# Performance work log

Hardware: AMD Instinct MI355X
Metric: run time of the kernel (lower is better)

## Reference

```python
import jax, jax.numpy as jnp
import numpy as np

H = 64  # lstm_units
FORGET_BIAS = 1.0  # TF LSTMCell default


def setup_inputs() -> dict:
    key = jax.random.key(0)
    k1, k2, k3 = jax.random.split(key, 3)
    B, T = 256, 2048
    x = jax.random.normal(k1, (B, T, 1), dtype=jnp.float32)
    # Layer 1: LSTMCell(64), input dim 1 -> kernel [(1+64), 4*64]
    W1 = jax.random.normal(k2, (1 + H, 4 * H), dtype=jnp.float32) * 0.1
    b1 = jnp.zeros((4 * H,), dtype=jnp.float32)
    # Layer 2: LSTMCell(1), input dim 64 -> kernel [(64+1), 4*1]
    W2 = jax.random.normal(k3, (H + 1, 4), dtype=jnp.float32) * 0.1
    b2 = jnp.zeros((4,), dtype=jnp.float32)
    return {"x": x, "W1": W1, "b1": b1, "W2": W2, "b2": b2}


def _lstm_step(c, h, xt, W, b):
    # TF LSTMCell: gates from concat([x, h]) @ W + b, order i, j, f, o
    z = jnp.concatenate([xt, h], axis=-1) @ W + b
    i, j, f, o = jnp.split(z, 4, axis=-1)
    c_new = jax.nn.sigmoid(f + FORGET_BIAS) * c + jax.nn.sigmoid(i) * jnp.tanh(j)
    h_new = jax.nn.sigmoid(o) * jnpp_tanh(c_new) if False else jax.nn.sigmoid(o) * jnp.tanh(c_new)
    return c_new, h_new


def reference(x, W1, b1, W2, b2):
    # x: [B, T, 1] -> outputs of 2-layer stacked LSTM, final layer size 1
    B = x.shape[0]

    def step(carry, xt):
        c1, h1, c2, h2 = carry
        c1, h1 = _lstm_step(c1, h1, xt, W1, b1)
        c2, h2 = _lstm_step(c2, h2, h1, W2, b2)
        return (c1, h1, c2, h2), h2

    init = (
        jnp.zeros((B, H), x.dtype),
        jnp.zeros((B, H), x.dtype),
        jnp.zeros((B, 1), x.dtype),
        jnp.zeros((B, 1), x.dtype),
    )
    x_tbf = jnp.swapaxes(x, 0, 1)  # [T, B, 1]
    _, ys = jax.lax.scan(step, init, x_tbf)  # ys: [T, B, 1]
    return jnp.swapaxes(ys, 0, 1)  # [B, T, 1]
```

## Files before the change

### kernel.cpp

```cpp
#include <hip/hip_runtime.h>

constexpr int kT = 2048;
constexpr int kB = 256;
constexpr int kH = 64;

typedef __attribute__((ext_vector_type(2))) float f32x2;
typedef __attribute__((ext_vector_type(4))) float f32x4;

__device__ __forceinline__ float fast_sig(float x) {
    return __builtin_amdgcn_rcpf(1.0f + __expf(-x));
}
__device__ __forceinline__ float fast_tanh(float x) {
    float t = __expf(2.0f * x);
    return 1.0f - 2.0f * __builtin_amdgcn_rcpf(t + 1.0f);
}

__global__ __launch_bounds__(128)
__attribute__((amdgpu_waves_per_eu(1, 1)))
void lstm2_kernel(
    const float* __restrict__ x, const float* __restrict__ W1,
    const float* __restrict__ b1, const float* __restrict__ W2,
    const float* __restrict__ b2, float* __restrict__ out)
{
    __shared__ f32x4 x4_lds[kT / 4];
    __shared__ f32x4 out4_lds[kT / 4];
    __shared__ float h_lds[2][kH];
    __shared__ f32x4 z4_lds[2];
    __shared__ float pad_lds[11128];

    float* x_lds = (float*)x4_lds;
    float* out_lds = (float*)out4_lds;

    const int tid = threadIdx.x;
    const int b = blockIdx.x;
    const int w = tid >> 6;
    const int l = tid & 63;
    const int p = l >> 5;
    const int u = w * 32 + (l & 31);

    const f32x4* xg4 = (const f32x4*)(x + (size_t)b * kT);
    f32x4* outg4 = (f32x4*)(out + (size_t)b * kT);

    for (int i = tid; i < kT / 4; i += 128) x4_lds[i] = xg4[i];
    if (tid < kH) { h_lds[0][tid] = 0.0f; h_lds[1][tid] = 0.0f; }
    if (b == 0x7fffffff) pad_lds[tid] = x[0];

    f32x2 wp[4][16];
    float w0g[4], bg[4];
    const int base = p * 32;
    #pragma unroll
    for (int g = 0; g < 4; ++g) {
        const int col = g * 64 + u;
        w0g[g] = W1[col];
        bg[g]  = b1[col];
        #pragma unroll
        for (int j = 0; j < 16; ++j) {
            wp[g][j].x = W1[(base + 2 * j + 1) * 256 + col];
            wp[g][j].y = W1[(base + 2 * j + 2) * 256 + col];
        }
    }
    const int s = l & 15, gg = l >> 4;
    float w2p0 = W2[(s +  0) * 4 + gg];
    float w2p1 = W2[(s + 16) * 4 + gg];
    float w2p2 = W2[(s + 32) * 4 + gg];
    float w2p3 = W2[(s + 48) * 4 + gg];
    float b2g  = b2[gg];
    f32x4 w2t = ((const f32x4*)W2)[kH];

    #pragma unroll
    for (int g = 0; g < 4; ++g) {
        #pragma unroll
        for (int j = 0; j < 16; ++j) asm volatile("" : "+v"(wp[g][j]));
        asm volatile("" : "+v"(w0g[g]), "+v"(bg[g]));
    }
    asm volatile("" : "+v"(w2p0), "+v"(w2p1), "+v"(w2p2), "+v"(w2p3));
    asm volatile("" : "+v"(w2t), "+v"(b2g));

    float c1 = 0.0f, c2 = 0.0f, h2 = 0.0f;

    __syncthreads();

    #pragma unroll 1
    for (int t = 0; t < kT; ++t) {
        const int cur = t & 1, nxt = cur ^ 1;

        const float xt = x_lds[t];
        f32x4 hp[8];
        const f32x4* hb4 = (const f32x4*)h_lds[cur];
        #pragma unroll
        for (int k = 0; k < 8; ++k) hp[k] = hb4[p * 8 + k];

        if (w == 0) {
            if (t >= 2) {
                const f32x4 z4 = z4_lds[nxt];
                const float zi = z4.x + h2 * w2t.x;
                const float zj = z4.y + h2 * w2t.y;
                const float zf = z4.z + h2 * w2t.z;
                const float zo = z4.w + h2 * w2t.w;
                c2 = fast_sig(zf + 1.0f) * c2 + fast_sig(zi) * fast_tanh(zj);
                h2 = fast_sig(zo) * fast_tanh(c2);
                if (l == 0) out_lds[t - 2] = h2;
            }
        } else {
            const float* hb = h_lds[cur];
            float pr = hb[s] * w2p0;
            pr = fmaf(hb[s + 16], w2p1, pr);
            pr = fmaf(hb[s + 32], w2p2, pr);
            pr = fmaf(hb[s + 48], w2p3, pr);
            pr += __shfl_xor(pr, 1);
            pr += __shfl_xor(pr, 2);
            pr += __shfl_xor(pr, 4);
            pr += __shfl_xor(pr, 8);
            if ((l & 15) == 0) ((float*)&z4_lds[cur])[gg] = pr + b2g;
        }

        f32x2 a0, a1, a2, a3;
        a0.x = (p == 0) ? fmaf(xt, w0g[0], bg[0]) : 0.0f; a0.y = 0.0f;
        a1.x = (p == 0) ? fmaf(xt, w0g[1], bg[1]) : 0.0f; a1.y = 0.0f;
        a2.x = (p == 0) ? fmaf(xt, w0g[2], bg[2]) : 0.0f; a2.y = 0.0f;
        a3.x = (p == 0) ? fmaf(xt, w0g[3], bg[3]) : 0.0f; a3.y = 0.0f;
        #pragma unroll
        for (int k = 0; k < 8; ++k) {
            const f32x2 lo = hp[k].xy;
            const f32x2 hi = hp[k].zw;
            a0 += lo * wp[0][2*k]; a0 += hi * wp[0][2*k+1];
            a1 += lo * wp[1][2*k]; a1 += hi * wp[1][2*k+1];
            a2 += lo * wp[2][2*k]; a2 += hi * wp[2][2*k+1];
            a3 += lo * wp[3][2*k]; a3 += hi * wp[3][2*k+1];
        }
        float zi = a0.x + a0.y; zi += __shfl_xor(zi, 32);
        float zj = a1.x + a1.y; zj += __shfl_xor(zj, 32);
        float zf = a2.x + a2.y; zf += __shfl_xor(zf, 32);
        float zo = a3.x + a3.y; zo += __shfl_xor(zo, 32);
        const float gi = fast_sig(zi);
        const float gj = fast_tanh(zj);
        const float gf = fast_sig(zf + 1.0f);
        const float go = fast_sig(zo);
        c1 = fmaf(gf, c1, gi * gj);
        const float h1n = go * fast_tanh(c1);
        if (p == 0) h_lds[nxt][u] = h1n;

        __syncthreads();
    }

    if (w == 0) {
        {
            const f32x4 z4 = z4_lds[1];
            const float zi = z4.x + h2 * w2t.x;
            const float zj = z4.y + h2 * w2t.y;
            const float zf = z4.z + h2 * w2t.z;
            const float zo = z4.w + h2 * w2t.w;
            c2 = fast_sig(zf + 1.0f) * c2 + fast_sig(zi) * fast_tanh(zj);
            h2 = fast_sig(zo) * fast_tanh(c2);
            if (l == 0) out_lds[kT - 2] = h2;
        }
        {
            const float* hb = h_lds[0];
            float pr = hb[s] * w2p0;
            pr = fmaf(hb[s + 16], w2p1, pr);
            pr = fmaf(hb[s + 32], w2p2, pr);
            pr = fmaf(hb[s + 48], w2p3, pr);
            pr += __shfl_xor(pr, 1);
            pr += __shfl_xor(pr, 2);
            pr += __shfl_xor(pr, 4);
            pr += __shfl_xor(pr, 8);
            const float prb = pr + b2g;
            const float zi = __shfl(prb,  0) + h2 * w2t.x;
            const float zj = __shfl(prb, 16) + h2 * w2t.y;
            const float zf = __shfl(prb, 32) + h2 * w2t.z;
            const float zo = __shfl(prb, 48) + h2 * w2t.w;
            c2 = fast_sig(zf + 1.0f) * c2 + fast_sig(zi) * fast_tanh(zj);
            h2 = fast_sig(zo) * fast_tanh(c2);
            if (l == 0) out_lds[kT - 1] = h2;
        }
    }

    __syncthreads();
    for (int i = tid; i < kT / 4; i += 128) outg4[i] = out4_lds[i];
}

extern "C" void kernel_launch(void* const* d_in, const int* in_sizes, int n_in,
                              void* d_out, int out_size, void* d_ws, size_t ws_size,
                              hipStream_t stream) {
    const float* x  = (const float*)d_in[0];
    const float* W1 = (const float*)d_in[1];
    const float* b1 = (const float*)d_in[2];
    const float* W2 = (const float*)d_in[3];
    const float* b2 = (const float*)d_in[4];
    float* out = (float*)d_out;
    lstm2_kernel<<<kB, 128, 0, stream>>>(x, W1, b1, W2, b2, out);
}
```

Measured before the change: 1.228 ms.

## Spread layer-1 gates over four waves with one gate column per thread

The block grows from 128 to 256 threads. Each thread now owns one gate column of layer 1 and computes its full 64-term dot product, instead of half of a dot product for all four gates. The four gate activations are merged into a single sigmoid (tanh is expressed through sigmoid) and then exchanged across lanes with shuffles. The aim is to halve the per-step FMA chain and the transcendental count on the serial recurrence. In exchange, every step now pays four cross-lane shuffles and a larger barrier across four waves. The layer-2 partial product moves to wave 3 and skips its unused first step, and the LDS padding allocation is removed.

```diff
diff --git a/kernel.cpp b/kernel.cpp
--- a/kernel.cpp
+++ b/kernel.cpp
@@ -15,7 +15,7 @@
     return 1.0f - 2.0f * __builtin_amdgcn_rcpf(t + 1.0f);
 }
 
-__global__ __launch_bounds__(128)
+__global__ __launch_bounds__(256)
 __attribute__((amdgpu_waves_per_eu(1, 1)))
 void lstm2_kernel(
     const float* __restrict__ x, const float* __restrict__ W1,
@@ -26,7 +26,6 @@
     __shared__ f32x4 out4_lds[kT / 4];
     __shared__ float h_lds[2][kH];
     __shared__ f32x4 z4_lds[2];
-    __shared__ float pad_lds[11128];
 
     float* x_lds = (float*)x4_lds;
     float* out_lds = (float*)out4_lds;
@@ -35,46 +34,35 @@
     const int b = blockIdx.x;
     const int w = tid >> 6;
     const int l = tid & 63;
-    const int p = l >> 5;
-    const int u = w * 32 + (l & 31);
+    const int g = l >> 4;
+    const int s = l & 15;
+    const int u = 16 * w + s;
+    const int col = g * 64 + u;
 
     const f32x4* xg4 = (const f32x4*)(x + (size_t)b * kT);
     f32x4* outg4 = (f32x4*)(out + (size_t)b * kT);
 
-    for (int i = tid; i < kT / 4; i += 128) x4_lds[i] = xg4[i];
+    for (int i = tid; i < kT / 4; i += 256) x4_lds[i] = xg4[i];
     if (tid < kH) { h_lds[0][tid] = 0.0f; h_lds[1][tid] = 0.0f; }
-    if (b == 0x7fffffff) pad_lds[tid] = x[0];
 
-    f32x2 wp[4][16];
-    float w0g[4], bg[4];
-    const int base = p * 32;
+    const float w0  = W1[col];
+    const float b1g = b1[col];
+    f32x2 wh[32];
     #pragma unroll
-    for (int g = 0; g < 4; ++g) {
-        const int col = g * 64 + u;
-        w0g[g] = W1[col];
-        bg[g]  = b1[col];
-        #pragma unroll
-        for (int j = 0; j < 16; ++j) {
-            wp[g][j].x = W1[(base + 2 * j + 1) * 256 + col];
-            wp[g][j].y = W1[(base + 2 * j + 2) * 256 + col];
-        }
+    for (int j = 0; j < 32; ++j) {
+        wh[j].x = W1[(2 * j + 1) * 256 + col];
+        wh[j].y = W1[(2 * j + 2) * 256 + col];
     }
-    const int s = l & 15, gg = l >> 4;
-    float w2p0 = W2[(s +  0) * 4 + gg];
-    float w2p1 = W2[(s + 16) * 4 + gg];
-    float w2p2 = W2[(s + 32) * 4 + gg];
-    float w2p3 = W2[(s + 48) * 4 + gg];
-    float b2g  = b2[gg];
+    const float w2p0 = W2[(s +  0) * 4 + g];
+    const float w2p1 = W2[(s + 16) * 4 + g];
+    const float w2p2 = W2[(s + 32) * 4 + g];
+    const float w2p3 = W2[(s + 48) * 4 + g];
+    const float b2g  = b2[g];
     f32x4 w2t = ((const f32x4*)W2)[kH];
 
     #pragma unroll
-    for (int g = 0; g < 4; ++g) {
-        #pragma unroll
-        for (int j = 0; j < 16; ++j) asm volatile("" : "+v"(wp[g][j]));
-        asm volatile("" : "+v"(w0g[g]), "+v"(bg[g]));
-    }
-    asm volatile("" : "+v"(w2p0), "+v"(w2p1), "+v"(w2p2), "+v"(w2p3));
-    asm volatile("" : "+v"(w2t), "+v"(b2g));
+    for (int j = 0; j < 32; ++j) asm volatile("" : "+v"(wh[j]));
+    asm volatile("" : "+v"(w2t));
 
     float c1 = 0.0f, c2 = 0.0f, h2 = 0.0f;
 
@@ -83,12 +71,7 @@
     #pragma unroll 1
     for (int t = 0; t < kT; ++t) {
         const int cur = t & 1, nxt = cur ^ 1;
-
         const float xt = x_lds[t];
-        f32x4 hp[8];
-        const f32x4* hb4 = (const f32x4*)h_lds[cur];
-        #pragma unroll
-        for (int k = 0; k < 8; ++k) hp[k] = hb4[p * 8 + k];
 
         if (w == 0) {
             if (t >= 2) {
@@ -101,44 +84,45 @@
                 h2 = fast_sig(zo) * fast_tanh(c2);
                 if (l == 0) out_lds[t - 2] = h2;
             }
-        } else {
-            const float* hb = h_lds[cur];
-            float pr = hb[s] * w2p0;
-            pr = fmaf(hb[s + 16], w2p1, pr);
-            pr = fmaf(hb[s + 32], w2p2, pr);
-            pr = fmaf(hb[s + 48], w2p3, pr);
-            pr += __shfl_xor(pr, 1);
-            pr += __shfl_xor(pr, 2);
-            pr += __shfl_xor(pr, 4);
-            pr += __shfl_xor(pr, 8);
-            if ((l & 15) == 0) ((float*)&z4_lds[cur])[gg] = pr + b2g;
+        } else if (w == 3) {
+            if (t >= 1) {
+                const float* hb = h_lds[cur];
+                float pr = hb[s] * w2p0;
+                pr = fmaf(hb[s + 16], w2p1, pr);
+                pr = fmaf(hb[s + 32], w2p2, pr);
+                pr = fmaf(hb[s + 48], w2p3, pr);
+                pr += __shfl_xor(pr, 1);
+                pr += __shfl_xor(pr, 2);
+                pr += __shfl_xor(pr, 4);
+                pr += __shfl_xor(pr, 8);
+                if (s == 0) ((float*)&z4_lds[cur])[g] = pr + b2g;
+            }
         }
 
-        f32x2 a0, a1, a2, a3;
-        a0.x = (p == 0) ? fmaf(xt, w0g[0], bg[0]) : 0.0f; a0.y = 0.0f;
-        a1.x = (p == 0) ? fmaf(xt, w0g[1], bg[1]) : 0.0f; a1.y = 0.0f;
-        a2.x = (p == 0) ? fmaf(xt, w0g[2], bg[2]) : 0.0f; a2.y = 0.0f;
-        a3.x = (p == 0) ? fmaf(xt, w0g[3], bg[3]) : 0.0f; a3.y = 0.0f;
+        const f32x4* hb4 = (const f32x4*)h_lds[cur];
+        f32x2 a0 = {fmaf(xt, w0, b1g), 0.0f};
+        f32x2 a1 = {0.0f, 0.0f}, a2 = {0.0f, 0.0f}, a3 = {0.0f, 0.0f};
         #pragma unroll
-        for (int k = 0; k < 8; ++k) {
-            const f32x2 lo = hp[k].xy;
-            const f32x2 hi = hp[k].zw;
-            a0 += lo * wp[0][2*k]; a0 += hi * wp[0][2*k+1];
-            a1 += lo * wp[1][2*k]; a1 += hi * wp[1][2*k+1];
-            a2 += lo * wp[2][2*k]; a2 += hi * wp[2][2*k+1];
-            a3 += lo * wp[3][2*k]; a3 += hi * wp[3][2*k+1];
+        for (int k = 0; k < 16; k += 2) {
+            const f32x4 hA = hb4[k];
+            const f32x4 hB = hb4[k + 1];
+            a0 += hA.xy * wh[2 * k];
+            a1 += hA.zw * wh[2 * k + 1];
+            a2 += hB.xy * wh[2 * k + 2];
+            a3 += hB.zw * wh[2 * k + 3];
         }
-        float zi = a0.x + a0.y; zi += __shfl_xor(zi, 32);
-        float zj = a1.x + a1.y; zj += __shfl_xor(zj, 32);
-        float zf = a2.x + a2.y; zf += __shfl_xor(zf, 32);
-        float zo = a3.x + a3.y; zo += __shfl_xor(zo, 32);
-        const float gi = fast_sig(zi);
-        const float gj = fast_tanh(zj);
-        const float gf = fast_sig(zf + 1.0f);
-        const float go = fast_sig(zo);
-        c1 = fmaf(gf, c1, gi * gj);
-        const float h1n = go * fast_tanh(c1);
-        if (p == 0) h_lds[nxt][u] = h1n;
+        const f32x2 bb = (a0 + a1) + (a2 + a3);
+        const float z = bb.x + bb.y;
+        const float zz = (g == 1) ? 2.0f * z : ((g == 2) ? z + 1.0f : z);
+        const float sg = fast_sig(zz);
+        const float a = (g == 1) ? fmaf(2.0f, sg, -1.0f) : sg;
+        const float ai = __shfl(a, s);
+        const float aj = __shfl(a, s + 16);
+        const float af = __shfl(a, s + 32);
+        const float ao = __shfl(a, s + 48);
+        c1 = fmaf(af, c1, ai * aj);
+        const float h1n = ao * fast_tanh(c1);
+        if (g == 0) h_lds[nxt][u] = h1n;
 
         __syncthreads();
     }
@@ -176,7 +160,7 @@
     }
 
     __syncthreads();
-    for (int i = tid; i < kT / 4; i += 128) outg4[i] = out4_lds[i];
+    for (int i = tid; i < kT / 4; i += 256) outg4[i] = out4_lds[i];
 }
 
 extern "C" void kernel_launch(void* const* d_in, const int* in_sizes, int n_in,
@@ -188,5 +172,5 @@
     const float* W2 = (const float*)d_in[3];
     const float* b2 = (const float*)d_in[4];
     float* out = (float*)d_out;
-    lstm2_kernel<<<kB, 128, 0, stream>>>(x, W1, b1, W2, b2, out);
+    lstm2_kernel<<<kB, 256, 0, stream>>>(x, W1, b1, W2, b2, out);
 }
```

Measured after the change: 1.276 ms. +3.9%, slower.
